# Kernel tuning notes

Hardware: AMD Instinct MI355X
Metric: run time of the kernel (lower is better)

## Reference

```python
import jax, jax.numpy as jnp
import numpy as np

B, T, I, H = 256, 2048, 64, 256


def setup_inputs() -> dict:
    key = jax.random.key(0)
    ks = jax.random.split(key, 8)
    s_ih = 1.0 / np.sqrt(H)
    return {
        "x": jax.random.normal(ks[0], (B, T, I), dtype=jnp.float32),
        "lengths": jax.random.randint(ks[1], (B,), 1, T + 1),  # in [1, T]
        "W_ih": jax.random.uniform(ks[2], (H, I), minval=-s_ih, maxval=s_ih),
        "W_hh": jax.random.uniform(ks[3], (H, H), minval=-s_ih, maxval=s_ih),
        "b_ih": jax.random.uniform(ks[4], (H,), minval=-s_ih, maxval=s_ih),
        "b_hh": jax.random.uniform(ks[5], (H,), minval=-s_ih, maxval=s_ih),
        "W_fc": jax.random.uniform(ks[6], (1, H), minval=-s_ih, maxval=s_ih),
        "b_fc": jax.random.uniform(ks[7], (1,), minval=-s_ih, maxval=s_ih),
    }


def reference(x, lengths, W_ih, W_hh, b_ih, b_hh, W_fc, b_fc):
    # Vanilla RNN (tanh), batch_first: h_t = tanh(x_t W_ih^T + b_ih + h_{t-1} W_hh^T + b_hh)
    batch = x.shape[0]
    h0 = jnp.zeros((batch, W_hh.shape[0]), dtype=x.dtype)
    # Precompute input projections for all timesteps in one big GEMM: [B, T, H]
    xp = jnp.einsum("bti,hi->bth", x, W_ih) + b_ih + b_hh

    def step(h, xt):  # xt: [B, H]
        h = jnp.tanh(xt + h @ W_hh.T)
        return h, h

    _, hs = jax.lax.scan(step, h0, jnp.swapaxes(xp, 0, 1))  # hs: [T, B, H]
    out = jnp.swapaxes(hs, 0, 1)  # [B, T, H]
    # Per-sample last valid timestep gather
    last = out[jnp.arange(batch), lengths - 1]  # [B, H]
    return last @ W_fc.T + b_fc  # [B, 1]
```

## Files before the change

### kernel.cpp

```cpp
#include <hip/hip_runtime.h>


static constexpr int nB = 256;
static constexpr int nT = 2048;
static constexpr int nI = 64;
static constexpr int nH = 256;
static constexpr int XBLK = 32;
static constexpr int THREADS = 256;

typedef _Float16 f16x8 __attribute__((ext_vector_type(8)));
typedef float f32x4 __attribute__((ext_vector_type(4)));

__device__ __forceinline__ float fast_tanh(float x) {
  float a = fabsf(x);
  float e = __expf(-2.0f * a);
  float r = (1.0f - e) / (1.0f + e);
  return copysignf(r, x);
}

__global__ __launch_bounds__(THREADS, 1)
void rnn_mfma4(const float* __restrict__ x, const int* __restrict__ lengths,
               const float* __restrict__ Wih, const float* __restrict__ Whh,
               const float* __restrict__ bih, const float* __restrict__ bhh,
               const float* __restrict__ Wfc, const float* __restrict__ bfc,
               float* __restrict__ out)
{
  __shared__ __align__(16) _Float16 hbuf[2][nH];
  __shared__ __align__(16) _Float16 xbuf[2][XBLK * nI];
  __shared__ float red[4];

  const int b   = blockIdx.x;
  const int tid = threadIdx.x;
  const int w   = tid >> 6;
  const int l   = tid & 63;
  const int q   = l >> 4;
  const int n   = l & 15;
  const int len = lengths[b];
  const float* xb = x + (size_t)b * nT * nI;

  f16x8 Ah[4][8];
  f16x8 Ax[4][2];
#pragma unroll
  for (int mt = 0; mt < 4; ++mt) {
    const int row = 64 * w + 16 * mt + n;
#pragma unroll
    for (int kt = 0; kt < 8; ++kt) {
      const float* src = Whh + row * nH + 32 * kt + 8 * q;
      f16x8 a;
#pragma unroll
      for (int j = 0; j < 8; ++j) a[j] = (_Float16)src[j];
      Ah[mt][kt] = a;
    }
#pragma unroll
    for (int kt = 0; kt < 2; ++kt) {
      const float* src = Wih + row * nI + 32 * kt + 8 * q;
      f16x8 a;
#pragma unroll
      for (int j = 0; j < 8; ++j) a[j] = (_Float16)src[j];
      Ax[mt][kt] = a;
    }
  }
  f32x4 bias[4];
#pragma unroll
  for (int mt = 0; mt < 4; ++mt)
#pragma unroll
    for (int r = 0; r < 4; ++r) {
      const int r0 = 64 * w + 16 * mt + 4 * q + r;
      bias[mt][r] = bih[r0] + bhh[r0];
    }
  const int mt_sel  = n >> 2;
  const int reg_sel = n & 3;
  const int row_own = 64 * w + 16 * mt_sel + 4 * q + reg_sel;

  hbuf[0][tid] = (_Float16)0.f;
  {
    float4 v0 = *(const float4*)(xb + tid * 8);
    float4 v1 = *(const float4*)(xb + tid * 8 + 4);
    f16x8 d = { (_Float16)v0.x, (_Float16)v0.y, (_Float16)v0.z, (_Float16)v0.w,
                (_Float16)v1.x, (_Float16)v1.y, (_Float16)v1.z, (_Float16)v1.w };
    *(f16x8*)(xbuf[0] + tid * 8) = d;
  }
  __syncthreads();

  int t = 0;
  for (int blk = 0; t < len; ++blk) {
    float4 pre0, pre1;
    const bool havepre = ((blk + 1) * XBLK < len);
    if (havepre) {
      const float* ps = xb + (size_t)(blk + 1) * XBLK * nI + tid * 8;
      pre0 = *(const float4*)ps;
      pre1 = *(const float4*)(ps + 4);
    }

    const int nsteps = min(XBLK, len - blk * XBLK);
    const _Float16* xB = xbuf[blk & 1];

    for (int s = 0; s < nsteps; ++s, ++t) {
      const _Float16* hsrc = hbuf[t & 1];
      const _Float16* xsrc = xB + s * nI;

      f32x4 acc0 = bias[0], acc1 = bias[1], acc2 = bias[2], acc3 = bias[3];
#pragma unroll
      for (int kt = 0; kt < 8; ++kt) {
        f16x8 Bh = *(const f16x8*)(hsrc + 32 * kt + 8 * q);
        acc0 = __builtin_amdgcn_mfma_f32_16x16x32_f16(Ah[0][kt], Bh, acc0, 0, 0, 0);
        acc1 = __builtin_amdgcn_mfma_f32_16x16x32_f16(Ah[1][kt], Bh, acc1, 0, 0, 0);
        acc2 = __builtin_amdgcn_mfma_f32_16x16x32_f16(Ah[2][kt], Bh, acc2, 0, 0, 0);
        acc3 = __builtin_amdgcn_mfma_f32_16x16x32_f16(Ah[3][kt], Bh, acc3, 0, 0, 0);
      }
#pragma unroll
      for (int kt = 0; kt < 2; ++kt) {
        f16x8 Bx = *(const f16x8*)(xsrc + 32 * kt + 8 * q);
        acc0 = __builtin_amdgcn_mfma_f32_16x16x32_f16(Ax[0][kt], Bx, acc0, 0, 0, 0);
        acc1 = __builtin_amdgcn_mfma_f32_16x16x32_f16(Ax[1][kt], Bx, acc1, 0, 0, 0);
        acc2 = __builtin_amdgcn_mfma_f32_16x16x32_f16(Ax[2][kt], Bx, acc2, 0, 0, 0);
        acc3 = __builtin_amdgcn_mfma_f32_16x16x32_f16(Ax[3][kt], Bx, acc3, 0, 0, 0);
      }

      f32x4 ax = (n & 4) ? acc1 : acc0;
      f32x4 ay = (n & 4) ? acc3 : acc2;
      f32x4 a  = (n & 8) ? ay : ax;
      float lo = (reg_sel & 1) ? a[1] : a[0];
      float hi = (reg_sel & 1) ? a[3] : a[2];
      float v  = (reg_sel & 2) ? hi : lo;
      float hn = fast_tanh(v);

      if (s == nsteps - 1 && havepre) {
        f16x8 d = { (_Float16)pre0.x, (_Float16)pre0.y, (_Float16)pre0.z, (_Float16)pre0.w,
                    (_Float16)pre1.x, (_Float16)pre1.y, (_Float16)pre1.z, (_Float16)pre1.w };
        *(f16x8*)(xbuf[(blk + 1) & 1] + tid * 8) = d;
      }
      hbuf[(t + 1) & 1][row_own] = (_Float16)hn;
      __syncthreads();
    }
  }

  float v = (float)hbuf[len & 1][tid] * Wfc[tid];
#pragma unroll
  for (int off = 32; off; off >>= 1) v += __shfl_down(v, off);
  if (l == 0) red[w] = v;
  __syncthreads();
  if (tid == 0) out[b] = ((red[0] + red[1]) + (red[2] + red[3])) + bfc[0];
}

extern "C" void kernel_launch(void* const* d_in, const int* in_sizes, int n_in,
                              void* d_out, int out_size, void* d_ws, size_t ws_size,
                              hipStream_t stream) {
  const float* x   = (const float*)d_in[0];
  const int* lens  = (const int*)d_in[1];
  const float* Wih = (const float*)d_in[2];
  const float* Whh = (const float*)d_in[3];
  const float* bih = (const float*)d_in[4];
  const float* bhh = (const float*)d_in[5];
  const float* Wfc = (const float*)d_in[6];
  const float* bfc = (const float*)d_in[7];
  float* out = (float*)d_out;

  rnn_mfma4<<<nB, THREADS, 0, stream>>>(x, lens, Wih, Whh, bih, bhh, Wfc, bfc, out);
}
```

Before: 1.453 ms.

## Pack four batch samples per block into MFMA N columns

Each workgroup now processes four sequences at once. The sample index is mapped onto the N dimension of the 16x16x32 MFMA, so the otherwise replicated B columns do useful work and the grid shrinks from 256 to 64 blocks. Each block runs to the longest of its four lengths and saves each sample's final hidden state in a separate LDS buffer. The x tile is shortened and padded, and the per-step barrier becomes an explicit lgkmcnt wait plus s_barrier. In exchange, each thread does four tanh evaluations and more LDS stores per step, and only a quarter of the CUs are used, while the sequential step count stays bounded by the longest sequence.

New measurement: 1.949 ms. 1.34x slower.

```diff
diff --git a/kernel.cpp b/kernel.cpp
--- a/kernel.cpp
+++ b/kernel.cpp
@@ -1,15 +1,23 @@
 #include <hip/hip_runtime.h>
 
 
-static constexpr int nB = 256;
 static constexpr int nT = 2048;
 static constexpr int nI = 64;
 static constexpr int nH = 256;
-static constexpr int XBLK = 32;
+static constexpr int SAMP = 4;
+static constexpr int XBLK = 16;
+static constexpr int HS = nH + 16;
+static constexpr int XS = nI + 16;
+static constexpr int XROW = SAMP * XS + 8;
 static constexpr int THREADS = 256;
 
 typedef _Float16 f16x8 __attribute__((ext_vector_type(8)));
+typedef _Float16 f16x4 __attribute__((ext_vector_type(4)));
 typedef float f32x4 __attribute__((ext_vector_type(4)));
+
+__device__ __forceinline__ void barrier_lgkm() {
+  asm volatile("s_waitcnt lgkmcnt(0)\n\ts_barrier" ::: "memory");
+}
 
 __device__ __forceinline__ float fast_tanh(float x) {
   float a = fabsf(x);
@@ -19,27 +27,33 @@
 }
 
 __global__ __launch_bounds__(THREADS, 1)
-void rnn_mfma4(const float* __restrict__ x, const int* __restrict__ lengths,
-               const float* __restrict__ Wih, const float* __restrict__ Whh,
-               const float* __restrict__ bih, const float* __restrict__ bhh,
-               const float* __restrict__ Wfc, const float* __restrict__ bfc,
-               float* __restrict__ out)
+void rnn_v6(const float* __restrict__ x, const int* __restrict__ lengths,
+            const float* __restrict__ Wih, const float* __restrict__ Whh,
+            const float* __restrict__ bih, const float* __restrict__ bhh,
+            const float* __restrict__ Wfc, const float* __restrict__ bfc,
+            float* __restrict__ out)
 {
-  __shared__ __align__(16) _Float16 hbuf[2][nH];
-  __shared__ __align__(16) _Float16 xbuf[2][XBLK * nI];
-  __shared__ float red[4];
-
-  const int b   = blockIdx.x;
+  __shared__ __align__(16) _Float16 hbuf[2][SAMP * HS];
+  __shared__ __align__(16) _Float16 hlast[SAMP * HS];
+  __shared__ __align__(16) _Float16 xbuf[2][XBLK * XROW];
+
+  const int b0  = blockIdx.x * SAMP;
   const int tid = threadIdx.x;
   const int w   = tid >> 6;
   const int l   = tid & 63;
   const int q   = l >> 4;
   const int n   = l & 15;
-  const int len = lengths[b];
-  const float* xb = x + (size_t)b * nT * nI;
+  const int sl  = n & 3;
+  const int grp = n >> 2;
+
+  const int len0 = lengths[b0 + 0], len1 = lengths[b0 + 1];
+  const int len2 = lengths[b0 + 2], len3 = lengths[b0 + 3];
+  const int maxlen = max(max(len0, len1), max(len2, len3));
+  const int mylen  = (sl == 0) ? len0 : (sl == 1) ? len1 : (sl == 2) ? len2 : len3;
 
   f16x8 Ah[4][8];
   f16x8 Ax[4][2];
+  f32x4 bias[4];
 #pragma unroll
   for (int mt = 0; mt < 4; ++mt) {
     const int row = 64 * w + 16 * mt + n;
@@ -59,50 +73,52 @@
       for (int j = 0; j < 8; ++j) a[j] = (_Float16)src[j];
       Ax[mt][kt] = a;
     }
-  }
-  f32x4 bias[4];
-#pragma unroll
-  for (int mt = 0; mt < 4; ++mt)
 #pragma unroll
     for (int r = 0; r < 4; ++r) {
-      const int r0 = 64 * w + 16 * mt + 4 * q + r;
-      bias[mt][r] = bih[r0] + bhh[r0];
-    }
-  const int mt_sel  = n >> 2;
-  const int reg_sel = n & 3;
-  const int row_own = 64 * w + 16 * mt_sel + 4 * q + reg_sel;
-
-  hbuf[0][tid] = (_Float16)0.f;
+      const int rr = 64 * w + 16 * mt + 4 * q + r;
+      bias[mt][r] = bih[rr] + bhh[rr];
+    }
+  }
+
+#pragma unroll
+  for (int sp = 0; sp < SAMP; ++sp) hbuf[0][sp * HS + tid] = (_Float16)0.f;
   {
-    float4 v0 = *(const float4*)(xb + tid * 8);
-    float4 v1 = *(const float4*)(xb + tid * 8 + 4);
-    f16x8 d = { (_Float16)v0.x, (_Float16)v0.y, (_Float16)v0.z, (_Float16)v0.w,
-                (_Float16)v1.x, (_Float16)v1.y, (_Float16)v1.z, (_Float16)v1.w };
-    *(f16x8*)(xbuf[0] + tid * 8) = d;
+    const int s_thr = tid >> 4;
+    const int i4    = (tid & 15) * 4;
+#pragma unroll
+    for (int sp = 0; sp < SAMP; ++sp) {
+      float4 v = *(const float4*)(x + ((size_t)(b0 + sp) * nT + s_thr) * nI + i4);
+      *(f16x4*)&xbuf[0][s_thr * XROW + sp * XS + i4] =
+          f16x4{ (_Float16)v.x, (_Float16)v.y, (_Float16)v.z, (_Float16)v.w };
+    }
   }
   __syncthreads();
 
   int t = 0;
-  for (int blk = 0; t < len; ++blk) {
-    float4 pre0, pre1;
-    const bool havepre = ((blk + 1) * XBLK < len);
-    if (havepre) {
-      const float* ps = xb + (size_t)(blk + 1) * XBLK * nI + tid * 8;
-      pre0 = *(const float4*)ps;
-      pre1 = *(const float4*)(ps + 4);
-    }
-
-    const int nsteps = min(XBLK, len - blk * XBLK);
-    const _Float16* xB = xbuf[blk & 1];
+  for (int blk = 0; t < maxlen; ++blk) {
+    const int t0n = (blk + 1) * XBLK;
+    const bool havenext = t0n < maxlen;
+    float4 pre[SAMP];
+    const int s_thr = tid >> 4;
+    const int i4    = (tid & 15) * 4;
+    if (havenext) {
+#pragma unroll
+      for (int sp = 0; sp < SAMP; ++sp)
+        pre[sp] = *(const float4*)(x + ((size_t)(b0 + sp) * nT + t0n + s_thr) * nI + i4);
+    }
+
+    const int nsteps = min(XBLK, maxlen - blk * XBLK);
+    const _Float16* xc = xbuf[blk & 1];
 
     for (int s = 0; s < nsteps; ++s, ++t) {
       const _Float16* hsrc = hbuf[t & 1];
-      const _Float16* xsrc = xB + s * nI;
+      _Float16*       hdst = hbuf[(t + 1) & 1];
 
       f32x4 acc0 = bias[0], acc1 = bias[1], acc2 = bias[2], acc3 = bias[3];
+
 #pragma unroll
       for (int kt = 0; kt < 8; ++kt) {
-        f16x8 Bh = *(const f16x8*)(hsrc + 32 * kt + 8 * q);
+        f16x8 Bh = *(const f16x8*)(hsrc + sl * HS + 32 * kt + 8 * q);
         acc0 = __builtin_amdgcn_mfma_f32_16x16x32_f16(Ah[0][kt], Bh, acc0, 0, 0, 0);
         acc1 = __builtin_amdgcn_mfma_f32_16x16x32_f16(Ah[1][kt], Bh, acc1, 0, 0, 0);
         acc2 = __builtin_amdgcn_mfma_f32_16x16x32_f16(Ah[2][kt], Bh, acc2, 0, 0, 0);
@@ -110,37 +126,71 @@
       }
 #pragma unroll
       for (int kt = 0; kt < 2; ++kt) {
-        f16x8 Bx = *(const f16x8*)(xsrc + 32 * kt + 8 * q);
+        f16x8 Bx = *(const f16x8*)(xc + s * XROW + sl * XS + 32 * kt + 8 * q);
         acc0 = __builtin_amdgcn_mfma_f32_16x16x32_f16(Ax[0][kt], Bx, acc0, 0, 0, 0);
         acc1 = __builtin_amdgcn_mfma_f32_16x16x32_f16(Ax[1][kt], Bx, acc1, 0, 0, 0);
         acc2 = __builtin_amdgcn_mfma_f32_16x16x32_f16(Ax[2][kt], Bx, acc2, 0, 0, 0);
         acc3 = __builtin_amdgcn_mfma_f32_16x16x32_f16(Ax[3][kt], Bx, acc3, 0, 0, 0);
       }
 
-      f32x4 ax = (n & 4) ? acc1 : acc0;
-      f32x4 ay = (n & 4) ? acc3 : acc2;
-      f32x4 a  = (n & 8) ? ay : ax;
-      float lo = (reg_sel & 1) ? a[1] : a[0];
-      float hi = (reg_sel & 1) ? a[3] : a[2];
-      float v  = (reg_sel & 2) ? hi : lo;
-      float hn = fast_tanh(v);
-
-      if (s == nsteps - 1 && havepre) {
-        f16x8 d = { (_Float16)pre0.x, (_Float16)pre0.y, (_Float16)pre0.z, (_Float16)pre0.w,
-                    (_Float16)pre1.x, (_Float16)pre1.y, (_Float16)pre1.z, (_Float16)pre1.w };
-        *(f16x8*)(xbuf[(blk + 1) & 1] + tid * 8) = d;
-      }
-      hbuf[(t + 1) & 1][row_own] = (_Float16)hn;
-      __syncthreads();
-    }
-  }
-
-  float v = (float)hbuf[len & 1][tid] * Wfc[tid];
-#pragma unroll
-  for (int off = 32; off; off >>= 1) v += __shfl_down(v, off);
-  if (l == 0) red[w] = v;
+      float v0, v1, v2, v3;
+      {
+        float a01 = (grp & 1) ? acc0[1] : acc0[0];
+        float a23 = (grp & 1) ? acc0[3] : acc0[2];
+        v0 = (grp & 2) ? a23 : a01;
+        a01 = (grp & 1) ? acc1[1] : acc1[0];
+        a23 = (grp & 1) ? acc1[3] : acc1[2];
+        v1 = (grp & 2) ? a23 : a01;
+        a01 = (grp & 1) ? acc2[1] : acc2[0];
+        a23 = (grp & 1) ? acc2[3] : acc2[2];
+        v2 = (grp & 2) ? a23 : a01;
+        a01 = (grp & 1) ? acc3[1] : acc3[0];
+        a23 = (grp & 1) ? acc3[3] : acc3[2];
+        v3 = (grp & 2) ? a23 : a01;
+      }
+      const _Float16 h0 = (_Float16)fast_tanh(v0);
+      const _Float16 h1 = (_Float16)fast_tanh(v1);
+      const _Float16 h2 = (_Float16)fast_tanh(v2);
+      const _Float16 h3 = (_Float16)fast_tanh(v3);
+
+      const int rbase = 64 * w + 4 * q + grp;
+      hdst[sl * HS + rbase]      = h0;
+      hdst[sl * HS + rbase + 16] = h1;
+      hdst[sl * HS + rbase + 32] = h2;
+      hdst[sl * HS + rbase + 48] = h3;
+
+      if (t + 1 == mylen) {
+        hlast[sl * HS + rbase]      = h0;
+        hlast[sl * HS + rbase + 16] = h1;
+        hlast[sl * HS + rbase + 32] = h2;
+        hlast[sl * HS + rbase + 48] = h3;
+      }
+
+      if (s == nsteps - 1 && havenext) {
+        _Float16* xd = xbuf[(blk + 1) & 1];
+#pragma unroll
+        for (int sp = 0; sp < SAMP; ++sp)
+          *(f16x4*)&xd[s_thr * XROW + sp * XS + i4] =
+              f16x4{ (_Float16)pre[sp].x, (_Float16)pre[sp].y,
+                     (_Float16)pre[sp].z, (_Float16)pre[sp].w };
+      }
+
+      barrier_lgkm();
+    }
+  }
+
   __syncthreads();
-  if (tid == 0) out[b] = ((red[0] + red[1]) + (red[2] + red[3])) + bfc[0];
+  {
+    float v = 0.f;
+#pragma unroll
+    for (int j = 0; j < 4; ++j) {
+      const int row = l + 64 * j;
+      v += (float)hlast[w * HS + row] * Wfc[row];
+    }
+#pragma unroll
+    for (int off = 32; off; off >>= 1) v += __shfl_down(v, off);
+    if (l == 0) out[b0 + w] = v + bfc[0];
+  }
 }
 
 extern "C" void kernel_launch(void* const* d_in, const int* in_sizes, int n_in,
@@ -156,5 +206,5 @@
   const float* bfc = (const float*)d_in[7];
   float* out = (float*)d_out;
 
-  rnn_mfma4<<<nB, THREADS, 0, stream>>>(x, lens, Wih, Whh, bih, bhh, Wfc, bfc, out);
-}
+  rnn_v6<<<256 / SAMP, THREADS, 0, stream>>>(x, lens, Wih, Whh, bih, bhh, Wfc, bfc, out);
+}
```
